# Kernel tuning notes

Hardware: AMD Instinct MI355X
Metric: run time of the kernel (lower is better)

Reference implementation:

```python
import jax, jax.numpy as jnp
import numpy as np

B, L, DIN, DQ, DS, DP = 16, 2048, 1024, 128, 64, 32

def _lin(k, din, dout):
    k1, k2 = jax.random.split(k)
    s = 1.0 / np.sqrt(din)
    W = jax.random.uniform(k1, (din, dout), jnp.float32, -s, s)
    b = jax.random.uniform(k2, (dout,), jnp.float32, -s, s)
    return W, b

def setup_inputs() -> dict:
    key = jax.random.key(0)
    ks = jax.random.split(key, 13)
    Wq, bq = _lin(ks[0], DIN, DQ)
    Wk, bk = _lin(ks[1], DIN, DQ)
    Wv, bv = _lin(ks[2], DIN, DQ)
    W1, b1 = _lin(ks[3], DS + DP, 128)
    W2, b2 = _lin(ks[4], 128, DQ)
    Wqc, bqc = _lin(ks[5], DQ, DQ)
    Wkc, bkc = _lin(ks[6], DQ, DQ)
    return dict(
        query=jax.random.normal(ks[7], (B, L, DIN), jnp.float32),
        key=jax.random.normal(ks[8], (B, L, DIN), jnp.float32),
        value=jax.random.normal(ks[9], (B, L, DIN), jnp.float32),
        sf=jax.random.normal(ks[10], (B, DS), jnp.float32),
        pos=jax.random.normal(ks[11], (L, DP), jnp.float32),
        Wq=Wq, bq=bq, Wk=Wk, bk=bk, Wv=Wv, bv=bv,
        W1=W1, b1=b1, W2=W2, b2=b2,
        Wqc=Wqc, bqc=bqc, Wkc=Wkc, bkc=bkc,
    )

def reference(query, key, value, sf, pos,
              Wq, bq, Wk, bk, Wv, bv,
              W1, b1, W2, b2, Wqc, bqc, Wkc, bkc):
    b, l, _ = query.shape
    q = query @ Wq + bq            # [b, l, dq]
    k = key @ Wk + bk              # [b, l, dq]
    v = value @ Wv + bv            # [b, l, dq]
    # CPE bias branch (pos is not None)
    sf_exp = jnp.broadcast_to(sf[:, None, :], (b, l, sf.shape[1]))
    pos_exp = jnp.broadcast_to(pos[None, :, :], (b, l, pos.shape[1]))
    cpe = jnp.concatenate([sf_exp, pos_exp], axis=2)         # [b, l, ds+32]
    cpe = jax.nn.relu(cpe @ W1 + b1) @ W2 + b2               # [b, l, dq]
    qc = cpe @ Wqc + bqc
    kc = cpe @ Wkc + bkc
    bias = jnp.einsum('bld,bmd->blm', qc, kc)                # [b, l, l]
    # add_mode == 0: post-softmax additive bias
    scale = jnp.sqrt(jnp.asarray(q.shape[-1], q.dtype))
    scores = jnp.einsum('bld,bmd->blm', q, k) / scale
    attn = jax.nn.softmax(scores, axis=-1) + bias
    out = jnp.einsum('blm,bmd->bld', attn, v)
    # L1 diff-norm regularizer over bias (use_cls=False)
    norm3 = (jnp.sum(jnp.abs(bias[:, 1:, :] - bias[:, :-1, :])) +
             jnp.sum(jnp.abs(bias[:, :, 1:] - bias[:, :, :-1])))
    return out, norm3
```

## Files before the change

kernel.cpp:

```cpp
#include <hip/hip_runtime.h>
#include <hip/hip_bf16.h>

typedef __attribute__((ext_vector_type(8))) short short8;
typedef __attribute__((ext_vector_type(4))) short short4x;
typedef __attribute__((ext_vector_type(4))) float floatx4;

#define MFMA16(a,b,c) __builtin_amdgcn_mfma_f32_16x16x32_bf16((a),(b),(c),0,0,0)

__device__ __forceinline__ unsigned short f2bf(float f) {
  unsigned int x = __float_as_uint(f);
  return (unsigned short)((x + 0x7fffu + ((x >> 16) & 1u)) >> 16);
}
__device__ __forceinline__ float bf2f(unsigned short s) {
  return __uint_as_float(((unsigned int)s) << 16);
}

__global__ __launch_bounds__(256)
void prep_kernel(const float* __restrict__ Wq, const float* __restrict__ Wk,
                 const float* __restrict__ Wv, const float* __restrict__ W1,
                 const float* __restrict__ b1, const float* __restrict__ W2,
                 const float* __restrict__ b2, const float* __restrict__ Wqc,
                 const float* __restrict__ bqc, const float* __restrict__ Wkc,
                 const float* __restrict__ bkc, const float* __restrict__ sf,
                 const float* __restrict__ pos,
                 unsigned short* __restrict__ Wf, unsigned short* __restrict__ Ut,
                 float* __restrict__ cqck, float* __restrict__ Asf,
                 float* __restrict__ Ppos)
{
  int blk = blockIdx.x, t = threadIdx.x;
  if (blk < 24) {
    int mat = blk >> 3, cg = blk & 7;
    const float* W = (mat == 0) ? Wq : (mat == 1) ? Wk : Wv;
    int l = t & 63, jp = t >> 6;
    int col = cg * 16 + (l & 15);
    unsigned short* o = Wf + (size_t)mat * 131072 + (size_t)cg * 32 * 512 + l * 8 + jp * 2;
    for (int ks = 0; ks < 32; ++ks) {
      int k = ks * 32 + (l >> 4) * 8 + jp * 2;
      o[ks * 512 + 0] = f2bf(W[(size_t)k * 128 + col]);
      o[ks * 512 + 1] = f2bf(W[(size_t)(k + 1) * 128 + col]);
    }
  } else if (blk >= 384 && blk < 512) {
    int j = blk - 384;
    int k = t & 127;
    const float* Wc = (t < 128) ? Wqc : Wkc;
    float acc = 0.f;
    for (int h = 0; h < 128; ++h) acc += W2[k * 128 + h] * Wc[h * 128 + j];
    Ut[(size_t)((t < 128) ? j : 128 + j) * 128 + k] = f2bf(acc);
  } else if (blk == 512) {
    int j = t & 127;
    const float* Wc = (t < 128) ? Wqc : Wkc;
    const float* bc = (t < 128) ? bqc : bkc;
    float acc = bc[j];
    for (int k = 0; k < 128; ++k) acc += b2[k] * Wc[k * 128 + j];
    cqck[t] = acc;
  } else if (blk > 512 && blk < 529) {
    int b = blk - 513;
    if (t < 128) {
      float acc = 0.f;
      for (int i = 0; i < 64; ++i) acc += sf[b * 64 + i] * W1[i * 128 + t];
      Asf[b * 128 + t] = acc;
    }
  } else if (blk >= 529) {
    int l = blk - 529;
    if (t < 128) {
      float acc = b1[t];
      for (int i = 0; i < 32; ++i) acc += pos[l * 32 + i] * W1[(64 + i) * 128 + t];
      Ppos[l * 128 + t] = acc;
    }
  }
}

__global__ __launch_bounds__(256)
void proj_kernel(const float* __restrict__ Xq, const float* __restrict__ Xk,
                 const float* __restrict__ Xv, const unsigned short* __restrict__ Wf3,
                 const float* __restrict__ bq, const float* __restrict__ bk,
                 const float* __restrict__ bv,
                 unsigned short* __restrict__ qo, unsigned short* __restrict__ ko,
                 unsigned short* __restrict__ vto)
{
  int which = blockIdx.y;
  const float* X = (which == 0) ? Xq : (which == 1) ? Xk : Xv;
  const unsigned short* Wf = Wf3 + (size_t)which * 131072;
  const float* bias = (which == 0) ? bq : (which == 1) ? bk : bv;

  __shared__ __align__(16) unsigned short X_lds[32 * 1032];

  int t = threadIdx.x;
  int w = t >> 6, l = t & 63;
  int rowbase = blockIdx.x * 32;
  const int lrow = l & 15, hi = l >> 4;

#pragma unroll
  for (int r = 0; r < 8; ++r) {
    int row = w * 8 + r;
    const float* src = X + (size_t)(rowbase + row) * 1024 + l * 4;
    unsigned short* dst = &X_lds[row * 1032 + l * 4];
#pragma unroll
    for (int i = 0; i < 4; ++i) {
      float4 v = *(const float4*)(src + i * 256);
      short4x s;
      s[0] = (short)f2bf(v.x); s[1] = (short)f2bf(v.y);
      s[2] = (short)f2bf(v.z); s[3] = (short)f2bf(v.w);
      *(short4x*)(dst + i * 256) = s;
    }
  }
  __syncthreads();

  const unsigned short* wp0 = Wf + (size_t)(w * 2) * 32 * 512 + l * 8;
  const unsigned short* wp1 = Wf + (size_t)(w * 2 + 1) * 32 * 512 + l * 8;
  const int xo0 = lrow * 1032 + hi * 8;
  const int xo1 = (lrow + 16) * 1032 + hi * 8;

  floatx4 acc[2][2];
#pragma unroll
  for (int i = 0; i < 2; ++i)
#pragma unroll
    for (int j = 0; j < 2; ++j) { acc[i][j][0]=0.f; acc[i][j][1]=0.f; acc[i][j][2]=0.f; acc[i][j][3]=0.f; }

#pragma unroll 4
  for (int ks = 0; ks < 32; ++ks) {
    short8 b0 = *(const short8*)(wp0 + ks * 512);
    short8 b1 = *(const short8*)(wp1 + ks * 512);
    short8 a0 = *(const short8*)&X_lds[xo0 + ks * 32];
    short8 a1 = *(const short8*)&X_lds[xo1 + ks * 32];
    acc[0][0] = MFMA16(a0, b0, acc[0][0]);
    acc[0][1] = MFMA16(a0, b1, acc[0][1]);
    acc[1][0] = MFMA16(a1, b0, acc[1][0]);
    acc[1][1] = MFMA16(a1, b1, acc[1][1]);
  }

#pragma unroll
  for (int mf = 0; mf < 2; ++mf)
#pragma unroll
    for (int nf = 0; nf < 2; ++nf) {
      int col = w * 32 + nf * 16 + lrow;
      float bb = bias[col];
#pragma unroll
      for (int j = 0; j < 4; ++j) {
        int grow = rowbase + mf * 16 + hi * 4 + j;
        float v = acc[mf][nf][j] + bb;
        if (which == 0) qo[(size_t)grow * 128 + col] = f2bf(v);
        else if (which == 1) ko[(size_t)grow * 128 + col] = f2bf(v);
        else {
          int b = grow >> 11, li = grow & 2047;
          vto[((size_t)b * 128 + col) * 2048 + li] = f2bf(v);
        }
      }
    }
}

__global__ __launch_bounds__(256)
void qckc_kernel(const float* __restrict__ Asf, const float* __restrict__ Ppos,
                 const unsigned short* __restrict__ Ut, const float* __restrict__ cqck,
                 unsigned short* __restrict__ qc, unsigned short* __restrict__ kc)
{
  __shared__ __align__(16) unsigned short hid[64 * 136];
  int t = threadIdx.x, w = t >> 6, l = t & 63;
  int lbase = blockIdx.x * 64;
  int b = lbase >> 11;
  const int lrow = l & 15, lk = (l >> 4) * 8;
  {
    int r = t >> 2, seg = (t & 3) * 32;
    const float* pp = Ppos + (size_t)((lbase + r) & 2047) * 128 + seg;
    const float* aa = Asf + b * 128 + seg;
    unsigned short* dst = hid + r * 136 + seg;
#pragma unroll
    for (int c = 0; c < 32; c += 4) {
      float4 p4 = *(const float4*)(pp + c);
      float4 a4 = *(const float4*)(aa + c);
      dst[c + 0] = f2bf(fmaxf(p4.x + a4.x, 0.f));
      dst[c + 1] = f2bf(fmaxf(p4.y + a4.y, 0.f));
      dst[c + 2] = f2bf(fmaxf(p4.z + a4.z, 0.f));
      dst[c + 3] = f2bf(fmaxf(p4.w + a4.w, 0.f));
    }
  }
  __syncthreads();
  short8 a[4];
#pragma unroll
  for (int ks = 0; ks < 4; ++ks)
    a[ks] = *(const short8*)&hid[(w * 16 + lrow) * 136 + ks * 32 + lk];
  floatx4 acc[16];
#pragma unroll
  for (int nf = 0; nf < 16; ++nf) { acc[nf][0]=0.f; acc[nf][1]=0.f; acc[nf][2]=0.f; acc[nf][3]=0.f; }
#pragma unroll
  for (int nf = 0; nf < 16; ++nf)
#pragma unroll
    for (int ks = 0; ks < 4; ++ks) {
      short8 bfr = *(const short8*)(Ut + (size_t)(nf * 16 + lrow) * 128 + ks * 32 + lk);
      acc[nf] = MFMA16(a[ks], bfr, acc[nf]);
    }
#pragma unroll
  for (int nf = 0; nf < 16; ++nf) {
    int col = nf * 16 + lrow;
    float bb = cqck[col];
#pragma unroll
    for (int j = 0; j < 4; ++j) {
      int grow = lbase + w * 16 + (l >> 4) * 4 + j;
      float v = acc[nf][j] + bb;
      if (col < 128) qc[(size_t)grow * 128 + col] = f2bf(v);
      else kc[(size_t)grow * 128 + (col - 128)] = f2bf(v);
    }
  }
}

__global__ __launch_bounds__(256)
void m2_partial_kernel(const unsigned short* __restrict__ vt,
                       const unsigned short* __restrict__ kc,
                       float* __restrict__ M2p)
{
  __shared__ __align__(16) unsigned short kct[128 * 40];
  int ks = blockIdx.x, b = blockIdx.y;
  int t = threadIdx.x, w = t >> 6, l = t & 63;
  const int lrow = l & 15, lk = (l >> 4) * 8;
  floatx4 acc[2][8];
#pragma unroll
  for (int i = 0; i < 2; ++i)
#pragma unroll
    for (int j = 0; j < 8; ++j) { acc[i][j][0]=0.f; acc[i][j][1]=0.f; acc[i][j][2]=0.f; acc[i][j][3]=0.f; }
  for (int mc = 0; mc < 8; ++mc) {
    int mbase = ks * 256 + mc * 32;
    {
      int mm = t & 31, ib = (t >> 5) * 16;
      const unsigned short* src = kc + ((size_t)b * 2048 + mbase + mm) * 128 + ib;
#pragma unroll
      for (int ii = 0; ii < 16; ++ii) kct[(ib + ii) * 40 + mm] = src[ii];
    }
    __syncthreads();
#pragma unroll
    for (int mf = 0; mf < 2; ++mf) {
      int jrow = w * 32 + mf * 16 + lrow;
      short8 a = *(const short8*)(vt + ((size_t)b * 128 + jrow) * 2048 + mbase + lk);
#pragma unroll
      for (int nf = 0; nf < 8; ++nf) {
        short8 bfr = *(const short8*)&kct[(nf * 16 + lrow) * 40 + lk];
        acc[mf][nf] = MFMA16(a, bfr, acc[mf][nf]);
      }
    }
    __syncthreads();
  }
#pragma unroll
  for (int mf = 0; mf < 2; ++mf)
#pragma unroll
    for (int nf = 0; nf < 8; ++nf)
#pragma unroll
      for (int j = 0; j < 4; ++j) {
        int jr = w * 32 + mf * 16 + (l >> 4) * 4 + j;
        int ic = nf * 16 + lrow;
        M2p[(((size_t)ks * 16 + b) * 128 + jr) * 128 + ic] = acc[mf][nf][j];
      }
}

__global__ void m2_reduce_kernel(const float* __restrict__ M2p, float* __restrict__ M2t)
{
  int idx = blockIdx.x * 256 + threadIdx.x;
  float s = 0.f;
#pragma unroll
  for (int ksp = 0; ksp < 8; ++ksp) s += M2p[(size_t)ksp * 262144 + idx];
  M2t[idx] = s;
}

__global__ __launch_bounds__(256)
void attn_kernel(const unsigned short* __restrict__ qbf, const unsigned short* __restrict__ kbf,
                 const unsigned short* __restrict__ vt, const unsigned short* __restrict__ qc,
                 const float* __restrict__ M2t, float* __restrict__ out)
{
  __shared__ __align__(16) unsigned short K_lds[64 * 136];
  __shared__ __align__(16) unsigned short V_lds[128 * 72];
  __shared__ __align__(16) unsigned short P_lds[4 * 16 * 72];
  int t = threadIdx.x, w = t >> 6, l = t & 63;
  int lbase = blockIdx.x * 64, b = blockIdx.y;
  const int lrow = l & 15, lk = (l >> 4) * 8;
  const float rscale = 0.08838834764831845f;

  size_t browq = (size_t)b * 2048 + lbase + w * 16 + lrow;
  short8 aq[4];
#pragma unroll
  for (int ks = 0; ks < 4; ++ks)
    aq[ks] = *(const short8*)(qbf + browq * 128 + ks * 32 + lk);

  float m_run[4] = {-1e30f, -1e30f, -1e30f, -1e30f};
  float s_run[4] = {0.f, 0.f, 0.f, 0.f};
  floatx4 o[8];
#pragma unroll
  for (int nf = 0; nf < 8; ++nf) { o[nf][0]=0.f; o[nf][1]=0.f; o[nf][2]=0.f; o[nf][3]=0.f; }

  int sr = t >> 2, sseg = (t & 3) * 32;
  int vr = t >> 1, vseg = (t & 1) * 32;

  for (int kt = 0; kt < 32; ++kt) {
    int mbase = kt * 64;
    {
      const short8* src = (const short8*)(kbf + ((size_t)b * 2048 + mbase + sr) * 128 + sseg);
      short8* dst = (short8*)&K_lds[sr * 136 + sseg];
      dst[0] = src[0]; dst[1] = src[1]; dst[2] = src[2]; dst[3] = src[3];
      const short8* vsrc = (const short8*)(vt + ((size_t)b * 128 + vr) * 2048 + mbase + vseg);
      short8* vdst = (short8*)&V_lds[vr * 72 + vseg];
      vdst[0] = vsrc[0]; vdst[1] = vsrc[1]; vdst[2] = vsrc[2]; vdst[3] = vsrc[3];
    }
    __syncthreads();
    floatx4 s[4];
#pragma unroll
    for (int cf = 0; cf < 4; ++cf) {
      floatx4 a4; a4[0]=0.f; a4[1]=0.f; a4[2]=0.f; a4[3]=0.f;
#pragma unroll
      for (int ks = 0; ks < 4; ++ks) {
        short8 bfr = *(const short8*)&K_lds[(cf * 16 + lrow) * 136 + ks * 32 + lk];
        a4 = MFMA16(aq[ks], bfr, a4);
      }
      s[cf] = a4 * rscale;
    }
    float fmul[4];
#pragma unroll
    for (int j = 0; j < 4; ++j) {
      float tm = fmaxf(fmaxf(s[0][j], s[1][j]), fmaxf(s[2][j], s[3][j]));
#pragma unroll
      for (int off = 1; off < 16; off <<= 1) tm = fmaxf(tm, __shfl_xor(tm, off, 64));
      float nm = fmaxf(m_run[j], tm);
      float f = __expf(m_run[j] - nm);
      m_run[j] = nm;
      float rs = 0.f;
#pragma unroll
      for (int cf = 0; cf < 4; ++cf) {
        float p = __expf(s[cf][j] - nm);
        s[cf][j] = p;
        rs += p;
      }
#pragma unroll
      for (int off = 1; off < 16; off <<= 1) rs += __shfl_xor(rs, off, 64);
      s_run[j] = s_run[j] * f + rs;
      fmul[j] = f;
    }
#pragma unroll
    for (int nf = 0; nf < 8; ++nf)
#pragma unroll
      for (int j = 0; j < 4; ++j) o[nf][j] *= fmul[j];
    unsigned short* pw = P_lds + w * (16 * 72);
#pragma unroll
    for (int cf = 0; cf < 4; ++cf)
#pragma unroll
      for (int j = 0; j < 4; ++j)
        pw[((l >> 4) * 4 + j) * 72 + cf * 16 + lrow] = f2bf(s[cf][j]);
#pragma unroll
    for (int kf = 0; kf < 2; ++kf) {
      short8 ap = *(const short8*)&pw[lrow * 72 + kf * 32 + lk];
#pragma unroll
      for (int nf = 0; nf < 8; ++nf) {
        short8 bv = *(const short8*)&V_lds[(nf * 16 + lrow) * 72 + kf * 32 + lk];
        o[nf] = MFMA16(ap, bv, o[nf]);
      }
    }
    __syncthreads();
  }
#pragma unroll
  for (int nf = 0; nf < 8; ++nf)
#pragma unroll
    for (int j = 0; j < 4; ++j) o[nf][j] /= s_run[j];
#pragma unroll
  for (int ks = 0; ks < 4; ++ks) {
    short8 aqc = *(const short8*)(qc + browq * 128 + ks * 32 + lk);
#pragma unroll
    for (int nf = 0; nf < 8; ++nf) {
      const float* mp = M2t + ((size_t)b * 128 + nf * 16 + lrow) * 128 + ks * 32 + lk;
      float4 m0 = *(const float4*)(mp);
      float4 m1 = *(const float4*)(mp + 4);
      short8 bm;
      bm[0]=(short)f2bf(m0.x); bm[1]=(short)f2bf(m0.y); bm[2]=(short)f2bf(m0.z); bm[3]=(short)f2bf(m0.w);
      bm[4]=(short)f2bf(m1.x); bm[5]=(short)f2bf(m1.y); bm[6]=(short)f2bf(m1.z); bm[7]=(short)f2bf(m1.w);
      o[nf] = MFMA16(aqc, bm, o[nf]);
    }
  }
#pragma unroll
  for (int nf = 0; nf < 8; ++nf)
#pragma unroll
    for (int j = 0; j < 4; ++j) {
      int grow = lbase + w * 16 + (l >> 4) * 4 + j;
      out[((size_t)b * 2048 + grow) * 128 + nf * 16 + lrow] = o[nf][j];
    }
}

__global__ __launch_bounds__(256)
void norm_kernel(const unsigned short* __restrict__ qc, const unsigned short* __restrict__ kc,
                 float* __restrict__ partial)
{
  __shared__ __align__(16) unsigned short T1[129 * 136];
  __shared__ __align__(16) unsigned short T2[129 * 136];
  __shared__ float red[8];
  int t = threadIdx.x, w = t >> 6, l = t & 63;
  int ltm = blockIdx.x;
  int lt = ltm >> 4, mt = ltm & 15;
  int b = blockIdx.y;
  const int lrow = l & 15, lk = (l >> 4) * 8;
  {
    int r = t >> 1, half = (t & 1) * 64;
    const unsigned short* asrc = qc + ((size_t)b * 2048 + lt * 128 + r) * 128 + half;
    const unsigned short* bsrc = kc + ((size_t)b * 2048 + mt * 128 + r) * 128 + half;
    unsigned short* adst = T1 + r * 136 + half;
    unsigned short* bdst = T2 + r * 136 + half;
#pragma unroll
    for (int c = 0; c < 64; c += 8) {
      *(short8*)(adst + c) = *(const short8*)(asrc + c);
      *(short8*)(bdst + c) = *(const short8*)(bsrc + c);
    }
    if (t < 16) {
      int gr = lt * 128 + 128; if (gr > 2047) gr = 2047;
      *(short8*)(T1 + 128 * 136 + t * 8) =
          *(const short8*)(qc + ((size_t)b * 2048 + gr) * 128 + t * 8);
    } else if (t < 32) {
      int c = (t - 16) * 8;
      int gr = mt * 128 + 128; if (gr > 2047) gr = 2047;
      *(short8*)(T2 + 128 * 136 + c) =
          *(const short8*)(kc + ((size_t)b * 2048 + gr) * 128 + c);
    }
  }
  __syncthreads();
  floatx4 acc0[2][8], acc1[2][8];
#pragma unroll
  for (int i = 0; i < 2; ++i)
#pragma unroll
    for (int j = 0; j < 8; ++j) {
      acc0[i][j][0]=0.f; acc0[i][j][1]=0.f; acc0[i][j][2]=0.f; acc0[i][j][3]=0.f;
      acc1[i][j][0]=0.f; acc1[i][j][1]=0.f; acc1[i][j][2]=0.f; acc1[i][j][3]=0.f;
    }
#pragma unroll
  for (int ks = 0; ks < 4; ++ks) {
    int off = ks * 32 + lk;
    short8 ad[2], cd[2];
#pragma unroll
    for (int mf = 0; mf < 2; ++mf) {
      int r = w * 32 + mf * 16 + lrow;
      short8 x1 = *(const short8*)&T1[r * 136 + off];
      short8 y1 = *(const short8*)&T1[(r + 1) * 136 + off];
      short8 x2 = *(const short8*)&T2[r * 136 + off];
      short8 y2 = *(const short8*)&T2[(r + 1) * 136 + off];
      short8 d1, d2;
#pragma unroll
      for (int ii = 0; ii < 8; ++ii) {
        d1[ii] = (short)f2bf(bf2f((unsigned short)y1[ii]) - bf2f((unsigned short)x1[ii]));
        d2[ii] = (short)f2bf(bf2f((unsigned short)y2[ii]) - bf2f((unsigned short)x2[ii]));
      }
      ad[mf] = d1; cd[mf] = d2;
    }
#pragma unroll
    for (int nf = 0; nf < 8; ++nf) {
      short8 bk = *(const short8*)&T2[(nf * 16 + lrow) * 136 + off];
      short8 bq = *(const short8*)&T1[(nf * 16 + lrow) * 136 + off];
      acc0[0][nf] = MFMA16(ad[0], bk, acc0[0][nf]);
      acc0[1][nf] = MFMA16(ad[1], bk, acc0[1][nf]);
      acc1[0][nf] = MFMA16(cd[0], bq, acc1[0][nf]);
      acc1[1][nf] = MFMA16(cd[1], bq, acc1[1][nf]);
    }
  }
  float s0 = 0.f, s1 = 0.f;
#pragma unroll
  for (int i = 0; i < 2; ++i)
#pragma unroll
    for (int nf = 0; nf < 8; ++nf)
#pragma unroll
      for (int j = 0; j < 4; ++j) {
        s0 += fabsf(acc0[i][nf][j]);
        s1 += fabsf(acc1[i][nf][j]);
      }
#pragma unroll
  for (int off = 1; off < 64; off <<= 1) {
    s0 += __shfl_xor(s0, off, 64);
    s1 += __shfl_xor(s1, off, 64);
  }
  if (l == 0) { red[w] = s0; red[4 + w] = s1; }
  __syncthreads();
  if (t == 0) {
    partial[((size_t)0 * 16 + b) * 256 + ltm] = red[0] + red[1] + red[2] + red[3];
    partial[((size_t)1 * 16 + b) * 256 + ltm] = red[4] + red[5] + red[6] + red[7];
  }
}

__global__ void norm_reduce_kernel(const float* __restrict__ partial, float* __restrict__ outp)
{
  __shared__ float red[4];
  int t = threadIdx.x;
  float s = 0.f;
  for (int i = t; i < 8192; i += 256) s += partial[i];
#pragma unroll
  for (int off = 1; off < 64; off <<= 1) s += __shfl_xor(s, off, 64);
  if ((t & 63) == 0) red[t >> 6] = s;
  __syncthreads();
  if (t == 0) outp[0] = red[0] + red[1] + red[2] + red[3];
}

extern "C" void kernel_launch(void* const* d_in, const int* in_sizes, int n_in,
                              void* d_out, int out_size, void* d_ws, size_t ws_size,
                              hipStream_t stream)
{
  const float* query = (const float*)d_in[0];
  const float* key_  = (const float*)d_in[1];
  const float* value = (const float*)d_in[2];
  const float* sf    = (const float*)d_in[3];
  const float* pos   = (const float*)d_in[4];
  const float* Wq  = (const float*)d_in[5];  const float* bq  = (const float*)d_in[6];
  const float* Wk  = (const float*)d_in[7];  const float* bk  = (const float*)d_in[8];
  const float* Wv  = (const float*)d_in[9];  const float* bv  = (const float*)d_in[10];
  const float* W1  = (const float*)d_in[11]; const float* b1  = (const float*)d_in[12];
  const float* W2  = (const float*)d_in[13]; const float* b2  = (const float*)d_in[14];
  const float* Wqc = (const float*)d_in[15]; const float* bqc = (const float*)d_in[16];
  const float* Wkc = (const float*)d_in[17]; const float* bkc = (const float*)d_in[18];
  float* out = (float*)d_out;

  char* ws = (char*)d_ws;
  size_t off = 0;
  auto alloc = [&](size_t bytes) {
    char* p = ws + off;
    off += (bytes + 255) & ~(size_t)255;
    return p;
  };
  unsigned short* Wf   = (unsigned short*)alloc((size_t)3 * 131072 * 2);
  unsigned short* Ut   = (unsigned short*)alloc((size_t)256 * 128 * 2);
  float* cqck          = (float*)alloc(256 * 4);
  float* Asf           = (float*)alloc(16 * 128 * 4);
  float* Ppos          = (float*)alloc((size_t)2048 * 128 * 4);
  unsigned short* qbf  = (unsigned short*)alloc((size_t)32768 * 128 * 2);
  unsigned short* kbf  = (unsigned short*)alloc((size_t)32768 * 128 * 2);
  unsigned short* vt   = (unsigned short*)alloc((size_t)32768 * 128 * 2);
  unsigned short* qc   = (unsigned short*)alloc((size_t)32768 * 128 * 2);
  unsigned short* kc   = (unsigned short*)alloc((size_t)32768 * 128 * 2);
  float* M2p           = (float*)alloc((size_t)8 * 262144 * 4);
  float* M2t           = (float*)alloc((size_t)262144 * 4);
  float* npartial      = (float*)alloc((size_t)8192 * 4);
  (void)ws_size; (void)in_sizes; (void)n_in; (void)out_size;

  prep_kernel<<<2577, 256, 0, stream>>>(Wq, Wk, Wv, W1, b1, W2, b2, Wqc, bqc, Wkc, bkc,
                                        sf, pos, Wf, Ut, cqck, Asf, Ppos);
  proj_kernel<<<dim3(1024, 3), 256, 0, stream>>>(query, key_, value, Wf, bq, bk, bv,
                                                 qbf, kbf, vt);
  qckc_kernel<<<512, 256, 0, stream>>>(Asf, Ppos, Ut, cqck, qc, kc);
  m2_partial_kernel<<<dim3(8, 16), 256, 0, stream>>>(vt, kc, M2p);
  m2_reduce_kernel<<<1024, 256, 0, stream>>>(M2p, M2t);
  attn_kernel<<<dim3(32, 16), 256, 0, stream>>>(qbf, kbf, vt, qc, M2t, out);
  norm_kernel<<<dim3(256, 16), 256, 0, stream>>>(qc, kc, npartial);
  norm_reduce_kernel<<<1, 256, 0, stream>>>(npartial, out + (size_t)4194304);
}
```

Measured before the change: 399.5 us.

## Prefetch K/V tiles into registers, use exp2 softmax, set MFMA priority

The attention loop now loads the next K and V tile into registers right after the barrier, so the global-memory latency overlaps with the current tile's compute. The score scale is folded with log2(e) so exp2f can replace __expf, and s_setprio raises wave priority around the MFMA sections. The projection launch is split into three separate kernel launches, one each for q, k and v, which removes the per-block pointer selection. The costs are extra registers for the prefetch buffers and two more kernel launches.

```diff
diff --git a/kernel.cpp b/kernel.cpp
--- a/kernel.cpp
+++ b/kernel.cpp
@@ -71,18 +71,11 @@
 }
 
 __global__ __launch_bounds__(256)
-void proj_kernel(const float* __restrict__ Xq, const float* __restrict__ Xk,
-                 const float* __restrict__ Xv, const unsigned short* __restrict__ Wf3,
-                 const float* __restrict__ bq, const float* __restrict__ bk,
-                 const float* __restrict__ bv,
+void proj_kernel(const float* __restrict__ X, const unsigned short* __restrict__ Wf,
+                 const float* __restrict__ bias,
                  unsigned short* __restrict__ qo, unsigned short* __restrict__ ko,
-                 unsigned short* __restrict__ vto)
-{
-  int which = blockIdx.y;
-  const float* X = (which == 0) ? Xq : (which == 1) ? Xk : Xv;
-  const unsigned short* Wf = Wf3 + (size_t)which * 131072;
-  const float* bias = (which == 0) ? bq : (which == 1) ? bk : bv;
-
+                 unsigned short* __restrict__ vto, int which)
+{
   __shared__ __align__(16) unsigned short X_lds[32 * 1032];
 
   int t = threadIdx.x;
@@ -270,7 +263,7 @@
   int t = threadIdx.x, w = t >> 6, l = t & 63;
   int lbase = blockIdx.x * 64, b = blockIdx.y;
   const int lrow = l & 15, lk = (l >> 4) * 8;
-  const float rscale = 0.08838834764831845f;
+  const float rscale2 = 0.08838834764831845f * 1.4426950408889634f;
 
   size_t browq = (size_t)b * 2048 + lbase + w * 16 + lrow;
   short8 aq[4];
@@ -287,18 +280,29 @@
   int sr = t >> 2, sseg = (t & 3) * 32;
   int vr = t >> 1, vseg = (t & 1) * 32;
 
+  const short8* ksrc0 = (const short8*)(kbf + ((size_t)b * 2048 + sr) * 128 + sseg);
+  const short8* vsrc0 = (const short8*)(vt + ((size_t)b * 128 + vr) * 2048 + vseg);
+
+  short8 kr[4], vrg[4];
+#pragma unroll
+  for (int i = 0; i < 4; ++i) { kr[i] = ksrc0[i]; vrg[i] = vsrc0[i]; }
+
   for (int kt = 0; kt < 32; ++kt) {
-    int mbase = kt * 64;
     {
-      const short8* src = (const short8*)(kbf + ((size_t)b * 2048 + mbase + sr) * 128 + sseg);
       short8* dst = (short8*)&K_lds[sr * 136 + sseg];
-      dst[0] = src[0]; dst[1] = src[1]; dst[2] = src[2]; dst[3] = src[3];
-      const short8* vsrc = (const short8*)(vt + ((size_t)b * 128 + vr) * 2048 + mbase + vseg);
+      dst[0] = kr[0]; dst[1] = kr[1]; dst[2] = kr[2]; dst[3] = kr[3];
       short8* vdst = (short8*)&V_lds[vr * 72 + vseg];
-      vdst[0] = vsrc[0]; vdst[1] = vsrc[1]; vdst[2] = vsrc[2]; vdst[3] = vsrc[3];
+      vdst[0] = vrg[0]; vdst[1] = vrg[1]; vdst[2] = vrg[2]; vdst[3] = vrg[3];
     }
     __syncthreads();
+    if (kt < 31) {
+      const short8* ks2 = ksrc0 + (size_t)(kt + 1) * 1024;
+      const short8* vs2 = vsrc0 + (size_t)(kt + 1) * 8;
+#pragma unroll
+      for (int i = 0; i < 4; ++i) { kr[i] = ks2[i]; vrg[i] = vs2[i]; }
+    }
     floatx4 s[4];
+    __builtin_amdgcn_s_setprio(1);
 #pragma unroll
     for (int cf = 0; cf < 4; ++cf) {
       floatx4 a4; a4[0]=0.f; a4[1]=0.f; a4[2]=0.f; a4[3]=0.f;
@@ -307,8 +311,9 @@
         short8 bfr = *(const short8*)&K_lds[(cf * 16 + lrow) * 136 + ks * 32 + lk];
         a4 = MFMA16(aq[ks], bfr, a4);
       }
-      s[cf] = a4 * rscale;
-    }
+      s[cf] = a4 * rscale2;
+    }
+    __builtin_amdgcn_s_setprio(0);
     float fmul[4];
 #pragma unroll
     for (int j = 0; j < 4; ++j) {
@@ -316,12 +321,12 @@
 #pragma unroll
       for (int off = 1; off < 16; off <<= 1) tm = fmaxf(tm, __shfl_xor(tm, off, 64));
       float nm = fmaxf(m_run[j], tm);
-      float f = __expf(m_run[j] - nm);
+      float f = exp2f(m_run[j] - nm);
       m_run[j] = nm;
       float rs = 0.f;
 #pragma unroll
       for (int cf = 0; cf < 4; ++cf) {
-        float p = __expf(s[cf][j] - nm);
+        float p = exp2f(s[cf][j] - nm);
         s[cf][j] = p;
         rs += p;
       }
@@ -340,6 +345,7 @@
 #pragma unroll
       for (int j = 0; j < 4; ++j)
         pw[((l >> 4) * 4 + j) * 72 + cf * 16 + lrow] = f2bf(s[cf][j]);
+    __builtin_amdgcn_s_setprio(1);
 #pragma unroll
     for (int kf = 0; kf < 2; ++kf) {
       short8 ap = *(const short8*)&pw[lrow * 72 + kf * 32 + lk];
@@ -349,6 +355,7 @@
         o[nf] = MFMA16(ap, bv, o[nf]);
       }
     }
+    __builtin_amdgcn_s_setprio(0);
     __syncthreads();
   }
 #pragma unroll
@@ -528,8 +535,9 @@
 
   prep_kernel<<<2577, 256, 0, stream>>>(Wq, Wk, Wv, W1, b1, W2, b2, Wqc, bqc, Wkc, bkc,
                                         sf, pos, Wf, Ut, cqck, Asf, Ppos);
-  proj_kernel<<<dim3(1024, 3), 256, 0, stream>>>(query, key_, value, Wf, bq, bk, bv,
-                                                 qbf, kbf, vt);
+  proj_kernel<<<1024, 256, 0, stream>>>(query, Wf,          bq, qbf, kbf, vt, 0);
+  proj_kernel<<<1024, 256, 0, stream>>>(key_,  Wf + 131072, bk, qbf, kbf, vt, 1);
+  proj_kernel<<<1024, 256, 0, stream>>>(value, Wf + 262144, bv, qbf, kbf, vt, 2);
   qckc_kernel<<<512, 256, 0, stream>>>(Asf, Ppos, Ut, cqck, qc, kc);
   m2_partial_kernel<<<dim3(8, 16), 256, 0, stream>>>(vt, kc, M2p);
   m2_reduce_kernel<<<1024, 256, 0, stream>>>(M2p, M2t);
```

After: 368.3 us. 1.08x faster.
